# Optimization experiments

Measured on AMD Instinct MI355X. Metric: run time of the kernel, lower is better.

## Reference

```python
import jax, jax.numpy as jnp
import numpy as np

TAU = 0.07          # temperature
TOP_N_SIM = 5       # n_neighb for KNN label assignment
RANKING_K = 4       # top-k same/diff-class sims for confidence ratio


def setup_inputs() -> dict:
    key = jax.random.key(0)
    k1, k2, k3 = jax.random.split(key, 3)
    n_src, n_tgt, d, n_cls = 8192, 6144, 256, 64
    return {
        "source_features": jax.random.normal(k1, (n_src, d), dtype=jnp.float32),
        "source_labels": jax.random.randint(k2, (n_src,), 0, n_cls, dtype=jnp.int32),
        "target_features": jax.random.normal(k3, (n_tgt, d), dtype=jnp.float32),
    }


def _l2_normalize(x):
    # F.normalize(x, dim=1, p=2) with eps=1e-12
    n = jnp.sqrt(jnp.sum(x * x, axis=1, keepdims=True))
    return x / jnp.maximum(n, 1e-12)


def reference(source_features, source_labels, target_features):
    n_tgt = target_features.shape[0]
    top_ranked_n = n_tgt * 2 // 3

    # cosine similarity matrix [n_src, n_tgt]
    sim = _l2_normalize(source_features) @ _l2_normalize(target_features).T

    # sort each column descending over sources
    order = jnp.argsort(-sim, axis=0)                      # [S, T]

    # KNN label assignment with torch.mode semantics (tie -> smallest value)
    neigh = source_labels[order[:TOP_N_SIM]]               # [K, T]
    counts = (neigh[:, None, :] == neigh[None, :, :]).sum(axis=1)  # [K, T]
    maxc = counts.max(axis=0)                              # [T]
    big = jnp.iinfo(source_labels.dtype).max
    assigned = jnp.where(counts == maxc[None, :], neigh, big).min(axis=0)  # [T]

    # sims & labels reordered by descending similarity, per column
    sorted_sims = jnp.take_along_axis(sim, order, axis=0)  # [S, T]
    sorted_labels = source_labels[order]                   # [S, T]
    pos = sorted_labels == assigned[None, :]               # [S, T]

    def first_k_masked_sum(mask):
        # sum of first RANKING_K sorted sims where mask is True, per column
        csum = jnp.cumsum(mask.astype(sim.dtype), axis=0)
        sel = mask & (csum <= RANKING_K)
        return jnp.sum(jnp.where(sel, sorted_sims, 0.0), axis=0)

    nln = first_k_masked_sum(pos)
    nun = first_k_masked_sum(~pos)
    scores = jax.lax.stop_gradient(nln / nun)              # [T], detached

    _, top_ind = jax.lax.top_k(scores, top_ranked_n)       # confident targets
    conf_sim = sim[:, top_ind]                             # [S, top_ranked_n]
    conf_lab = assigned[top_ind]

    # contrastive softmax loss over sources
    mask_sim = (source_labels[:, None] == conf_lab[None, :]).astype(sim.dtype)
    exp_scores = jax.nn.softmax(conf_sim / TAU, axis=0)
    contrastive = (exp_scores * mask_sim).sum(axis=0) / exp_scores.sum(axis=0)
    return -jnp.mean(jnp.log(contrastive + 1e-6))
```

## Files before the change

kernel.cpp:

```cpp
#include <hip/hip_runtime.h>
#include <cstdint>
#include <cstddef>

#define DIM 256
#define NSRC 8192
#define NTGT 6144
#define NCLS 64
#define KSTEPS 8
#define INV_TAU (1.0f / 0.07f)
#define EPITCH 136

typedef __attribute__((ext_vector_type(8))) short bf16x8;
typedef __attribute__((ext_vector_type(4))) float f32x4;
typedef unsigned char uchar;

__device__ __forceinline__ ushort f2bf_rne(float f) {
    uint u = __float_as_uint(f);
    uint r = u + 0x7fff + ((u >> 16) & 1);
    return (ushort)(r >> 16);
}
__device__ __forceinline__ uint bf2ord(uint u) {
    return u ^ (0x8000u + (u >> 15) * 0x7FFFu);
}
__device__ __forceinline__ float ord2f(uint o) {
    uint u = (o & 0x8000u) ? (o ^ 0x8000u) : (~o & 0xFFFFu);
    return __uint_as_float(u << 16);
}
__device__ __forceinline__ uint med3u(uint a, uint b, uint c) {
    uint d;
    asm("v_med3_u32 %0, %1, %2, %3" : "=v"(d) : "v"(a), "v"(b), "v"(c));
    return d;
}

__device__ __forceinline__ void gload_lds16(const void* g, void* l) {
    __builtin_amdgcn_global_load_lds((const __attribute__((address_space(1))) void*)g,
                                     (__attribute__((address_space(3))) void*)l,
                                     16, 0, 0);
}

__global__ __launch_bounds__(256) void l2bf2_k(const float* __restrict__ inA,
                                               ushort* __restrict__ outA, int nA,
                                               const float* __restrict__ inB,
                                               ushort* __restrict__ outB, int nB) {
    const int w = (blockIdx.x * 256 + threadIdx.x) >> 6;
    const int lane = threadIdx.x & 63;
    if (w >= nA + nB) return;
    const float* in;
    ushort* out;
    int row;
    if (w < nA) { in = inA; out = outA; row = w; }
    else        { in = inB; out = outB; row = w - nA; }
    float4 v = *(const float4*)(in + (size_t)row * DIM + lane * 4);
    float ss = v.x * v.x + v.y * v.y + v.z * v.z + v.w * v.w;
#pragma unroll
    for (int d = 1; d < 64; d <<= 1) ss += __shfl_xor(ss, d);
    const float n = fmaxf(sqrtf(ss), 1e-12f);
    ushort4 o;
    o.x = f2bf_rne(v.x / n);
    o.y = f2bf_rne(v.y / n);
    o.z = f2bf_rne(v.z / n);
    o.w = f2bf_rne(v.w / n);
    *(ushort4*)(out + (size_t)row * DIM + lane * 4) = o;
}

__global__ __launch_bounds__(256) void class_build_k(const int* __restrict__ labels,
                                                     uchar* __restrict__ lab8,
                                                     int* __restrict__ cstart,
                                                     int* __restrict__ clist, int n) {
    const int c = blockIdx.x, t = threadIdx.x;
    const int g = c * 256 + t;
    if (g < n) lab8[g] = (uchar)labels[g];

    __shared__ int sl[256], se[256];
    const int per = n >> 8;
    const int i0 = t * per;
    int less = 0, eq = 0;
    for (int j = 0; j < per; ++j) {
        const int l = labels[i0 + j];
        less += (l < c);
        eq += (l == c);
    }
    sl[t] = less; se[t] = eq;
    __syncthreads();
    for (int s = 1; s < 256; s <<= 1) {
        const int a = (t >= s) ? sl[t - s] : 0;
        const int b = (t >= s) ? se[t - s] : 0;
        __syncthreads();
        sl[t] += a; se[t] += b;
        __syncthreads();
    }
    const int base = sl[255];
    int pos = base + se[t] - eq;
    for (int j = 0; j < per; ++j) {
        const int i = i0 + j;
        if (labels[i] == c) clist[pos++] = i;
    }
    if (t == 0) cstart[c] = base;
    if (c == 0 && t == 1) cstart[NCLS] = n;
}

__global__ __launch_bounds__(256) void gemm_mfma_k(const ushort* __restrict__ A,
                                                   const ushort* __restrict__ B,
                                                   ushort* __restrict__ C,
                                                   float* __restrict__ s1p,
                                                   int M, int N) {
    __shared__ __align__(16) ushort smem[24576];

    const int tid = threadIdx.x;
    const int lane = tid & 63, wid = tid >> 6;
    const int wr = wid >> 1, wc = wid & 1;

    const int gx = gridDim.x;
    const int bid = blockIdx.y * gx + blockIdx.x;
    const int rowsPerX = gridDim.y >> 3;
    const int grpW = 8;
    const int grpSize = rowsPerX * grpW;
    const int xcd = bid & 7;
    const int local = bid >> 3;
    const int grp = local / grpSize;
    const int within = local % grpSize;
    const int bm = (xcd * rowsPerX + within % rowsPerX) * 128;
    const int bn = (grp * grpW + within / rowsPerX) * 128;

    const char* aSrc[2];
    const char* bSrc[2];
    uint ldsOff[2];
#pragma unroll
    for (int it = 0; it < 2; ++it) {
        const int c = it * 256 + tid;
        const int r = c >> 2;
        const int ch = c & 3;
        const int sch = ch ^ ((r >> 1) & 3);
        aSrc[it] = (const char*)A + (size_t)(bm + r) * (DIM * 2) + sch * 16;
        bSrc[it] = (const char*)B + (size_t)(bn + r) * (DIM * 2) + sch * 16;
        ldsOff[it] = it * 4096 + (uint)(wid * 1024);
    }

    const int fr = lane & 15, fk = lane >> 4;
    const int swz = (fr >> 1) & 3;
    int idxA[4], idxB[4];
#pragma unroll
    for (int m = 0; m < 4; ++m)
        idxA[m] = (wr * 64 + m * 16 + fr) * 32 + ((fk ^ swz) * 8);
#pragma unroll
    for (int n = 0; n < 4; ++n)
        idxB[n] = (wc * 64 + n * 16 + fr) * 32 + ((fk ^ swz) * 8);

    f32x4 acc[4][4];
#pragma unroll
    for (int m = 0; m < 4; ++m)
#pragma unroll
        for (int n = 0; n < 4; ++n) acc[m][n] = (f32x4){0.f, 0.f, 0.f, 0.f};

#define STAGE(b, ks)                                                               \
    {                                                                              \
        _Pragma("unroll") for (int it = 0; it < 2; ++it) {                         \
            gload_lds16(aSrc[it] + (ks) * 64,                                      \
                        (char*)smem + (b) * 8192 + ldsOff[it]);                    \
            gload_lds16(bSrc[it] + (ks) * 64,                                      \
                        (char*)smem + 24576 + (b) * 8192 + ldsOff[it]);            \
        }                                                                          \
    }

    STAGE(0, 0);
    STAGE(1, 1);

#pragma unroll
    for (int ks = 0; ks < KSTEPS; ++ks) {
        if (ks < KSTEPS - 1) { asm volatile("s_waitcnt vmcnt(4)" ::: "memory"); }
        else                 { asm volatile("s_waitcnt vmcnt(0)" ::: "memory"); }
        __builtin_amdgcn_s_barrier();
        asm volatile("" ::: "memory");

        if (ks + 2 < KSTEPS) STAGE((ks + 2) % 3, ks + 2);

        const int slot = ks % 3;
        const ushort* sAc = smem + slot * 4096;
        const ushort* sBc = smem + 12288 + slot * 4096;
        bf16x8 av[4], bv[4];
#pragma unroll
        for (int m = 0; m < 4; ++m) av[m] = *(const bf16x8*)&sAc[idxA[m]];
#pragma unroll
        for (int n = 0; n < 4; ++n) bv[n] = *(const bf16x8*)&sBc[idxB[n]];
#pragma unroll
        for (int m = 0; m < 4; ++m)
#pragma unroll
            for (int n = 0; n < 4; ++n)
                acc[m][n] = __builtin_amdgcn_mfma_f32_16x16x32_bf16(av[m], bv[n], acc[m][n], 0, 0, 0);
    }
#undef STAGE

    __syncthreads();
    {
        float rp[16];
#pragma unroll
        for (int m = 0; m < 4; ++m)
#pragma unroll
            for (int j = 0; j < 4; ++j) {
                float s = 0.f;
#pragma unroll
                for (int n = 0; n < 4; ++n) {
                    uint u = __float_as_uint(acc[m][n][j]);
                    uint ru = (u + 0x7fff + ((u >> 16) & 1)) & 0xFFFF0000u;
                    s += __expf(fmaf(__uint_as_float(ru), INV_TAU, -INV_TAU));
                }
                rp[m * 4 + j] = s;
            }
#pragma unroll
        for (int d = 1; d < 16; d <<= 1)
#pragma unroll
            for (int i = 0; i < 16; ++i) rp[i] += __shfl_xor(rp[i], d);
        float* s1red = (float*)((char*)smem + 34816);
        if (fr == 0) {
#pragma unroll
            for (int m = 0; m < 4; ++m)
#pragma unroll
                for (int j = 0; j < 4; ++j)
                    s1red[(wr * 64 + m * 16 + fk * 4 + j) * 2 + wc] = rp[m * 4 + j];
        }
    }
#pragma unroll
    for (int m = 0; m < 4; ++m) {
#pragma unroll
        for (int n = 0; n < 4; ++n) {
            const int colb = wc * 64 + n * 16 + fr;
#pragma unroll
            for (int j = 0; j < 4; ++j) {
                const int rowb = wr * 64 + m * 16 + fk * 4 + j;
                smem[rowb * EPITCH + colb] = (ushort)bf2ord((uint)f2bf_rne(acc[m][n][j]));
            }
        }
    }
    __syncthreads();
    if (tid < 128) {
        const float* s1red = (const float*)((const char*)smem + 34816);
        s1p[(size_t)(bn >> 7) * NTGT + bm + tid] = s1red[tid * 2] + s1red[tid * 2 + 1];
    }
    const int rr = tid >> 4, cc = (tid & 15) * 8;
#pragma unroll
    for (int it = 0; it < 8; ++it) {
        const int r = it * 16 + rr;
        uint4 v = *(const uint4*)&smem[r * EPITCH + cc];
        *(uint4*)(C + (size_t)(bm + r) * N + bn + cc) = v;
    }
}

__global__ __launch_bounds__(256) void assign_score_w(const ushort* __restrict__ sim,
                                                      const int* __restrict__ labels,
                                                      const uchar* __restrict__ lab8,
                                                      const int* __restrict__ cstart,
                                                      const int* __restrict__ clist,
                                                      const float* __restrict__ s1p,
                                                      float* __restrict__ scores_out,
                                                      float* __restrict__ logt_out) {
    const int lane = threadIdx.x & 63, wid = threadIdx.x >> 6;
    const int t = blockIdx.x * 4 + wid;
    const ushort* row = sim + (size_t)t * NSRC;

    uint k0 = 0, k1 = 0, k2 = 0, k3 = 0, k4 = 0, k5 = 0, k6 = 0, k7 = 0;

#define CH4(u16, idx)                                                   \
    {                                                                   \
        uint nk = (((uint)(u16)) << 16) | (uint)(8191 - (idx));         \
        uint q1 = med3u(nk, k0, k1);                                    \
        uint q2 = med3u(nk, k1, k2);                                    \
        uint q3 = med3u(nk, k2, k3);                                    \
        k0 = max(k0, nk); k1 = q1; k2 = q2; k3 = q3;                    \
    }
#define CH8(u16, idx)                                                   \
    {                                                                   \
        uint nk = (((uint)(u16)) << 16) | (uint)(8191 - (idx));         \
        uint q1 = med3u(nk, k0, k1);                                    \
        uint q2 = med3u(nk, k1, k2);                                    \
        uint q3 = med3u(nk, k2, k3);                                    \
        uint q4 = med3u(nk, k3, k4);                                    \
        uint q5 = med3u(nk, k4, k5);                                    \
        uint q6 = med3u(nk, k5, k6);                                    \
        uint q7 = med3u(nk, k6, k7);                                    \
        k0 = max(k0, nk);                                               \
        k1 = q1; k2 = q2; k3 = q3; k4 = q4; k5 = q5; k6 = q6; k7 = q7;  \
    }
#define MERGE8                                                                     \
    _Pragma("unroll")                                                              \
    for (int d = 1; d < 64; d <<= 1) {                                             \
        uint b0 = __shfl_xor(k0, d), b1 = __shfl_xor(k1, d), b2 = __shfl_xor(k2, d),\
             b3 = __shfl_xor(k3, d), b4 = __shfl_xor(k4, d), b5 = __shfl_xor(k5, d),\
             b6 = __shfl_xor(k6, d), b7 = __shfl_xor(k7, d);                        \
        uint r0 = max(k0, b0);                                                     \
        uint r1 = max(max(min(k0, b0), k1), b1);                                   \
        uint r2 = max(max(min(k0, b1), min(k1, b0)), max(k2, b2));                 \
        uint r3 = max(max(min(k0, b2), min(k1, b1)),                               \
                      max(max(min(k2, b0), k3), b3));                              \
        uint r4 = max(max(max(min(k0, b3), min(k1, b2)),                           \
                          max(min(k2, b1), min(k3, b0))), max(k4, b4));            \
        uint r5 = max(max(max(min(k0, b4), min(k1, b3)),                           \
                          max(min(k2, b2), min(k3, b1))),                          \
                      max(max(min(k4, b0), k5), b5));                              \
        uint r6 = max(max(max(min(k0, b5), min(k1, b4)),                           \
                          max(min(k2, b3), min(k3, b2))),                          \
                      max(max(min(k4, b1), min(k5, b0)), max(k6, b6)));            \
        uint r7 = max(max(max(min(k0, b6), min(k1, b5)),                           \
                          max(min(k2, b4), min(k3, b3))),                          \
                      max(max(min(k4, b2), min(k5, b1)),                           \
                          max(max(min(k6, b0), k7), b7)));                         \
        k0 = r0; k1 = r1; k2 = r2; k3 = r3; k4 = r4; k5 = r5; k6 = r6; k7 = r7;    \
    }

    for (int i0 = lane * 8; i0 < NSRC; i0 += 512) {
        uint4 w = *(const uint4*)(row + i0);
        CH4(w.x & 0xFFFF, i0 + 0); CH4(w.x >> 16, i0 + 1);
        CH4(w.y & 0xFFFF, i0 + 2); CH4(w.y >> 16, i0 + 3);
        CH4(w.z & 0xFFFF, i0 + 4); CH4(w.z >> 16, i0 + 5);
        CH4(w.w & 0xFFFF, i0 + 6); CH4(w.w >> 16, i0 + 7);
    }
    const uint prek3 = k3;
    MERGE8;
    if (!__all((int)(prek3 <= k7))) {
        k0 = k1 = k2 = k3 = k4 = k5 = k6 = k7 = 0;
        for (int i0 = lane * 8; i0 < NSRC; i0 += 512) {
            uint4 w = *(const uint4*)(row + i0);
            CH8(w.x & 0xFFFF, i0 + 0); CH8(w.x >> 16, i0 + 1);
            CH8(w.y & 0xFFFF, i0 + 2); CH8(w.y >> 16, i0 + 3);
            CH8(w.z & 0xFFFF, i0 + 4); CH8(w.z >> 16, i0 + 5);
            CH8(w.w & 0xFFFF, i0 + 6); CH8(w.w >> 16, i0 + 7);
        }
        MERGE8;
    }
#undef CH4
#undef CH8
#undef MERGE8

    float s1 = s1p[(size_t)lane * NTGT + t];
#pragma unroll
    for (int d = 1; d < 64; d <<= 1) s1 += __shfl_xor(s1, d);

    const int l0 = labels[8191 - (int)(k0 & 0xFFFF)];
    const int l1 = labels[8191 - (int)(k1 & 0xFFFF)];
    const int l2 = labels[8191 - (int)(k2 & 0xFFFF)];
    const int l3 = labels[8191 - (int)(k3 & 0xFFFF)];
    const int l4 = labels[8191 - (int)(k4 & 0xFFFF)];
    const int l5 = labels[8191 - (int)(k5 & 0xFFFF)];
    const int l6 = labels[8191 - (int)(k6 & 0xFFFF)];
    const int l7 = labels[8191 - (int)(k7 & 0xFFFF)];

    const int c0 = 1 + (l0 == l1) + (l0 == l2) + (l0 == l3) + (l0 == l4);
    const int c1 = (l1 == l0) + 1 + (l1 == l2) + (l1 == l3) + (l1 == l4);
    const int c2 = (l2 == l0) + (l2 == l1) + 1 + (l2 == l3) + (l2 == l4);
    const int c3 = (l3 == l0) + (l3 == l1) + (l3 == l2) + 1 + (l3 == l4);
    const int c4 = (l4 == l0) + (l4 == l1) + (l4 == l2) + (l4 == l3) + 1;
    const int maxc = max(max(max(c0, c1), max(c2, c3)), c4);
    int assigned = 0x7fffffff;
    if (c0 == maxc) assigned = min(assigned, l0);
    if (c1 == maxc) assigned = min(assigned, l1);
    if (c2 == maxc) assigned = min(assigned, l2);
    if (c3 == maxc) assigned = min(assigned, l3);
    if (c4 == maxc) assigned = min(assigned, l4);
    const int aL = assigned;

    const int negcnt = (l0 != aL) + (l1 != aL) + (l2 != aL) + (l3 != aL) +
                       (l4 != aL) + (l5 != aL) + (l6 != aL) + (l7 != aL);
    float nun = 0.f;
    if (negcnt >= 4) {
        int c = 0;
#define NSTEP(kj, lj)                                                       \
        {                                                                   \
            bool take = ((lj) != aL) && (c < 4);                            \
            nun += take ? ord2f((kj) >> 16) : 0.f;                          \
            c += take ? 1 : 0;                                              \
        }
        NSTEP(k0, l0) NSTEP(k1, l1) NSTEP(k2, l2) NSTEP(k3, l3)
        NSTEP(k4, l4) NSTEP(k5, l5) NSTEP(k6, l6) NSTEP(k7, l7)
#undef NSTEP
    } else {
        uint n0 = 0, n1 = 0, n2 = 0, n3 = 0;
        for (int i0 = lane * 8; i0 < NSRC; i0 += 512) {
            uint4 w = *(const uint4*)(row + i0);
            uint2 lw = *(const uint2*)(lab8 + i0);
#define NEGP(u16, lb)                                                       \
            {                                                               \
                uint x = ((lb) == aL) ? 0u : (uint)(u16);                   \
                uint q1 = med3u(x, n0, n1);                                 \
                uint q2 = med3u(x, n1, n2);                                 \
                uint q3 = med3u(x, n2, n3);                                 \
                n0 = max(n0, x); n1 = q1; n2 = q2; n3 = q3;                 \
            }
            NEGP(w.x & 0xFFFF, (int)(lw.x & 255));
            NEGP(w.x >> 16,    (int)((lw.x >> 8) & 255));
            NEGP(w.y & 0xFFFF, (int)((lw.x >> 16) & 255));
            NEGP(w.y >> 16,    (int)(lw.x >> 24));
            NEGP(w.z & 0xFFFF, (int)(lw.y & 255));
            NEGP(w.z >> 16,    (int)((lw.y >> 8) & 255));
            NEGP(w.w & 0xFFFF, (int)((lw.y >> 16) & 255));
            NEGP(w.w >> 16,    (int)(lw.y >> 24));
#undef NEGP
        }
#pragma unroll
        for (int d = 1; d < 64; d <<= 1) {
            uint b0 = __shfl_xor(n0, d), b1 = __shfl_xor(n1, d),
                 b2 = __shfl_xor(n2, d), b3 = __shfl_xor(n3, d);
            uint r0 = max(n0, b0);
            uint r1 = max(max(min(n0, b0), n1), b1);
            uint r2 = max(max(min(n0, b1), min(n1, b0)), max(n2, b2));
            uint r3 = max(max(min(n0, b2), min(n1, b1)),
                          max(max(min(n2, b0), n3), b3));
            n0 = r0; n1 = r1; n2 = r2; n3 = r3;
        }
        nun = (n0 ? ord2f(n0) : 0.f) + (n1 ? ord2f(n1) : 0.f) +
              (n2 ? ord2f(n2) : 0.f) + (n3 ? ord2f(n3) : 0.f);
    }

    const int cs = cstart[aL], ce = cstart[aL + 1];
    float tp0 = -2.f, tp1 = -2.f, tp2 = -2.f, tp3 = -2.f;
    float sp = 0.f;
    for (int p = cs + lane; p < ce; p += 64) {
        const int idx = clist[p];
        float v = ord2f((uint)row[idx]);
        sp += __expf(fmaf(v, INV_TAU, -INV_TAU));
        float q1 = __builtin_amdgcn_fmed3f(v, tp0, tp1);
        float q2 = __builtin_amdgcn_fmed3f(v, tp1, tp2);
        float q3 = __builtin_amdgcn_fmed3f(v, tp2, tp3);
        tp0 = fmaxf(tp0, v); tp1 = q1; tp2 = q2; tp3 = q3;
    }
#pragma unroll
    for (int d = 1; d < 64; d <<= 1) {
        sp += __shfl_xor(sp, d);
        float b0 = __shfl_xor(tp0, d), b1 = __shfl_xor(tp1, d),
              b2 = __shfl_xor(tp2, d), b3 = __shfl_xor(tp3, d);
        float r0 = fmaxf(tp0, b0);
        float r1 = fmaxf(fmaxf(fminf(tp0, b0), tp1), b1);
        float r2 = fmaxf(fmaxf(fminf(tp0, b1), fminf(tp1, b0)), fmaxf(tp2, b2));
        float r3 = fmaxf(fmaxf(fminf(tp0, b2), fminf(tp1, b1)),
                         fmaxf(fmaxf(fminf(tp2, b0), tp3), b3));
        tp0 = r0; tp1 = r1; tp2 = r2; tp3 = r3;
    }

    if (lane == 0) {
        float nln = (tp0 > -1.5f ? tp0 : 0.f) + (tp1 > -1.5f ? tp1 : 0.f) +
                    (tp2 > -1.5f ? tp2 : 0.f) + (tp3 > -1.5f ? tp3 : 0.f);
        scores_out[t] = nln / nun;
        logt_out[t] = logf(sp / s1 + 1e-6f);
    }
}

__global__ __launch_bounds__(256) void select_topk_w(const float* __restrict__ scores,
                                                     int* __restrict__ selected,
                                                     int n, int k) {
    const int lane = threadIdx.x & 63, wid = threadIdx.x >> 6;
    const int t = blockIdx.x * 4 + wid;
    if (t >= n) return;
    const float st = scores[t];
    int rank = 0;
    for (int j0 = lane * 4; j0 < n; j0 += 256) {
        float4 v = *(const float4*)(scores + j0);
        rank += (v.x > st) || (v.x == st && (j0 + 0) < t);
        rank += (v.y > st) || (v.y == st && (j0 + 1) < t);
        rank += (v.z > st) || (v.z == st && (j0 + 2) < t);
        rank += (v.w > st) || (v.w == st && (j0 + 3) < t);
    }
    for (int d = 1; d < 64; d <<= 1) rank += __shfl_xor(rank, d);
    if (lane == 0) selected[t] = (rank < k) ? 1 : 0;
}

__global__ __launch_bounds__(256) void finalize_k(const float* __restrict__ logt,
                                                  const int* __restrict__ selected,
                                                  float* __restrict__ out, int n, int k) {
    __shared__ float red[256];
    const int tid = threadIdx.x;
    float s = 0.f;
    for (int i = tid; i < n; i += 256) s += selected[i] ? logt[i] : 0.f;
    red[tid] = s;
    __syncthreads();
    for (int st = 128; st > 0; st >>= 1) {
        if (tid < st) red[tid] += red[tid + st];
        __syncthreads();
    }
    if (tid == 0) out[0] = -red[0] / (float)k;
}

extern "C" void kernel_launch(void* const* d_in, const int* in_sizes, int n_in,
                              void* d_out, int out_size, void* d_ws, size_t ws_size,
                              hipStream_t stream) {
    const float* srcF = (const float*)d_in[0];
    const int* labels = (const int*)d_in[1];
    const float* tgtF = (const float*)d_in[2];
    float* out = (float*)d_out;

    const int n_src = in_sizes[1];
    const int d = in_sizes[0] / n_src;
    const int n_tgt = in_sizes[2] / d;
    const int topn = n_tgt * 2 / 3;

    char* ws = (char*)d_ws;
    ushort* src2 = (ushort*)ws;  ws += (size_t)n_src * DIM * sizeof(ushort);
    ushort* tgt2 = (ushort*)ws;  ws += (size_t)n_tgt * DIM * sizeof(ushort);
    ushort* sim  = (ushort*)ws;  ws += (size_t)n_tgt * NSRC * sizeof(ushort);
    float* scores = (float*)ws;  ws += (size_t)n_tgt * sizeof(float);
    float* logt   = (float*)ws;  ws += (size_t)n_tgt * sizeof(float);
    int* selected = (int*)ws;    ws += (size_t)n_tgt * sizeof(int);
    int* cstart   = (int*)ws;    ws += (size_t)(NCLS + 1) * sizeof(int);
    int* clist    = (int*)ws;    ws += (size_t)n_src * sizeof(int);
    uchar* lab8   = (uchar*)ws;  ws += (size_t)n_src;
    ws = (char*)(((uintptr_t)ws + 255) & ~(uintptr_t)255);
    float* s1p    = (float*)ws;  ws += (size_t)64 * NTGT * sizeof(float);

    const int nrows = n_tgt + n_src;
    l2bf2_k<<<(nrows + 3) / 4, 256, 0, stream>>>(tgtF, tgt2, n_tgt, srcF, src2, n_src);
    class_build_k<<<NCLS, 256, 0, stream>>>(labels, lab8, cstart, clist, n_src);

    dim3 grid(n_src / 128, n_tgt / 128);
    gemm_mfma_k<<<grid, 256, 0, stream>>>(tgt2, src2, sim, s1p, n_tgt, n_src);

    assign_score_w<<<n_tgt / 4, 256, 0, stream>>>(sim, labels, lab8, cstart, clist,
                                                  s1p, scores, logt);
    select_topk_w<<<(n_tgt + 3) / 4, 256, 0, stream>>>(scores, selected, n_tgt, topn);
    finalize_k<<<1, 256, 0, stream>>>(logt, selected, out, n_tgt, topn);
}
```

Before: 128.3 us.

## Move exp-sum from GEMM epilogue into assign kernel, store raw bf16

Drops the per-tile exp-sum reduction and the s1p partial-sum buffer from the GEMM epilogue. The softmax denominator is now computed in the assign kernel while it already streams each row. The GEMM stores plain bf16 instead of order-preserving keys, and the key transform moves into the assign kernel's selection loops. The main loop now handles two independent 512-element chunks with separate top-4 lists that are merged afterwards, to raise ILP. This takes work off the GEMM epilogue and removes a global buffer, but the assign kernel must now do an exp and a key transform per element.

```diff
diff --git a/kernel.cpp b/kernel.cpp
--- a/kernel.cpp
+++ b/kernel.cpp
@@ -4,7 +4,6 @@
 
 #define DIM 256
 #define NSRC 8192
-#define NTGT 6144
 #define NCLS 64
 #define KSTEPS 8
 #define INV_TAU (1.0f / 0.07f)
@@ -102,7 +101,6 @@
 __global__ __launch_bounds__(256) void gemm_mfma_k(const ushort* __restrict__ A,
                                                    const ushort* __restrict__ B,
                                                    ushort* __restrict__ C,
-                                                   float* __restrict__ s1p,
                                                    int M, int N) {
     __shared__ __align__(16) ushort smem[24576];
 
@@ -191,34 +189,6 @@
 #undef STAGE
 
     __syncthreads();
-    {
-        float rp[16];
-#pragma unroll
-        for (int m = 0; m < 4; ++m)
-#pragma unroll
-            for (int j = 0; j < 4; ++j) {
-                float s = 0.f;
-#pragma unroll
-                for (int n = 0; n < 4; ++n) {
-                    uint u = __float_as_uint(acc[m][n][j]);
-                    uint ru = (u + 0x7fff + ((u >> 16) & 1)) & 0xFFFF0000u;
-                    s += __expf(fmaf(__uint_as_float(ru), INV_TAU, -INV_TAU));
-                }
-                rp[m * 4 + j] = s;
-            }
-#pragma unroll
-        for (int d = 1; d < 16; d <<= 1)
-#pragma unroll
-            for (int i = 0; i < 16; ++i) rp[i] += __shfl_xor(rp[i], d);
-        float* s1red = (float*)((char*)smem + 34816);
-        if (fr == 0) {
-#pragma unroll
-            for (int m = 0; m < 4; ++m)
-#pragma unroll
-                for (int j = 0; j < 4; ++j)
-                    s1red[(wr * 64 + m * 16 + fk * 4 + j) * 2 + wc] = rp[m * 4 + j];
-        }
-    }
 #pragma unroll
     for (int m = 0; m < 4; ++m) {
 #pragma unroll
@@ -227,15 +197,11 @@
 #pragma unroll
             for (int j = 0; j < 4; ++j) {
                 const int rowb = wr * 64 + m * 16 + fk * 4 + j;
-                smem[rowb * EPITCH + colb] = (ushort)bf2ord((uint)f2bf_rne(acc[m][n][j]));
+                smem[rowb * EPITCH + colb] = f2bf_rne(acc[m][n][j]);
             }
         }
     }
     __syncthreads();
-    if (tid < 128) {
-        const float* s1red = (const float*)((const char*)smem + 34816);
-        s1p[(size_t)(bn >> 7) * NTGT + bm + tid] = s1red[tid * 2] + s1red[tid * 2 + 1];
-    }
     const int rr = tid >> 4, cc = (tid & 15) * 8;
 #pragma unroll
     for (int it = 0; it < 8; ++it) {
@@ -250,26 +216,33 @@
                                                       const uchar* __restrict__ lab8,
                                                       const int* __restrict__ cstart,
                                                       const int* __restrict__ clist,
-                                                      const float* __restrict__ s1p,
                                                       float* __restrict__ scores_out,
                                                       float* __restrict__ logt_out) {
     const int lane = threadIdx.x & 63, wid = threadIdx.x >> 6;
     const int t = blockIdx.x * 4 + wid;
     const ushort* row = sim + (size_t)t * NSRC;
 
-    uint k0 = 0, k1 = 0, k2 = 0, k3 = 0, k4 = 0, k5 = 0, k6 = 0, k7 = 0;
-
-#define CH4(u16, idx)                                                   \
+    uint kA0 = 0, kA1 = 0, kA2 = 0, kA3 = 0;
+    uint kB0 = 0, kB1 = 0, kB2 = 0, kB3 = 0;
+    float s1a = 0.f, s1b = 0.f;
+
+#define CH4X(u16, idx, K0, K1, K2, K3, S1)                              \
     {                                                                   \
-        uint nk = (((uint)(u16)) << 16) | (uint)(8191 - (idx));         \
-        uint q1 = med3u(nk, k0, k1);                                    \
-        uint q2 = med3u(nk, k1, k2);                                    \
-        uint q3 = med3u(nk, k2, k3);                                    \
-        k0 = max(k0, nk); k1 = q1; k2 = q2; k3 = q3;                    \
+        uint uu = (uint)(u16);                                          \
+        float vv = __uint_as_float(uu << 16);                           \
+        S1 += __expf(fmaf(vv, INV_TAU, -INV_TAU));                      \
+        uint od = uu ^ (0x8000u + (uu >> 15) * 0x7FFFu);                \
+        uint nk = (od << 16) | (uint)(8191 - (idx));                    \
+        uint q1 = med3u(nk, K0, K1);                                    \
+        uint q2 = med3u(nk, K1, K2);                                    \
+        uint q3 = med3u(nk, K2, K3);                                    \
+        K0 = max(K0, nk); K1 = q1; K2 = q2; K3 = q3;                    \
     }
 #define CH8(u16, idx)                                                   \
     {                                                                   \
-        uint nk = (((uint)(u16)) << 16) | (uint)(8191 - (idx));         \
+        uint uu = (uint)(u16);                                          \
+        uint od = uu ^ (0x8000u + (uu >> 15) * 0x7FFFu);                \
+        uint nk = (od << 16) | (uint)(8191 - (idx));                    \
         uint q1 = med3u(nk, k0, k1);                                    \
         uint q2 = med3u(nk, k1, k2);                                    \
         uint q3 = med3u(nk, k2, k3);                                    \
@@ -306,13 +279,33 @@
         k0 = r0; k1 = r1; k2 = r2; k3 = r3; k4 = r4; k5 = r5; k6 = r6; k7 = r7;    \
     }
 
-    for (int i0 = lane * 8; i0 < NSRC; i0 += 512) {
+    for (int i0 = lane * 8; i0 < NSRC; i0 += 1024) {
         uint4 w = *(const uint4*)(row + i0);
-        CH4(w.x & 0xFFFF, i0 + 0); CH4(w.x >> 16, i0 + 1);
-        CH4(w.y & 0xFFFF, i0 + 2); CH4(w.y >> 16, i0 + 3);
-        CH4(w.z & 0xFFFF, i0 + 4); CH4(w.z >> 16, i0 + 5);
-        CH4(w.w & 0xFFFF, i0 + 6); CH4(w.w >> 16, i0 + 7);
-    }
+        uint4 w2 = *(const uint4*)(row + i0 + 512);
+        CH4X(w.x & 0xFFFF, i0 + 0, kA0, kA1, kA2, kA3, s1a);
+        CH4X(w.x >> 16,    i0 + 1, kA0, kA1, kA2, kA3, s1a);
+        CH4X(w.y & 0xFFFF, i0 + 2, kA0, kA1, kA2, kA3, s1a);
+        CH4X(w.y >> 16,    i0 + 3, kA0, kA1, kA2, kA3, s1a);
+        CH4X(w.z & 0xFFFF, i0 + 4, kA0, kA1, kA2, kA3, s1a);
+        CH4X(w.z >> 16,    i0 + 5, kA0, kA1, kA2, kA3, s1a);
+        CH4X(w.w & 0xFFFF, i0 + 6, kA0, kA1, kA2, kA3, s1a);
+        CH4X(w.w >> 16,    i0 + 7, kA0, kA1, kA2, kA3, s1a);
+        CH4X(w2.x & 0xFFFF, i0 + 512, kB0, kB1, kB2, kB3, s1b);
+        CH4X(w2.x >> 16,    i0 + 513, kB0, kB1, kB2, kB3, s1b);
+        CH4X(w2.y & 0xFFFF, i0 + 514, kB0, kB1, kB2, kB3, s1b);
+        CH4X(w2.y >> 16,    i0 + 515, kB0, kB1, kB2, kB3, s1b);
+        CH4X(w2.z & 0xFFFF, i0 + 516, kB0, kB1, kB2, kB3, s1b);
+        CH4X(w2.z >> 16,    i0 + 517, kB0, kB1, kB2, kB3, s1b);
+        CH4X(w2.w & 0xFFFF, i0 + 518, kB0, kB1, kB2, kB3, s1b);
+        CH4X(w2.w >> 16,    i0 + 519, kB0, kB1, kB2, kB3, s1b);
+    }
+    uint k0 = max(kA0, kB0);
+    uint k1 = max(max(min(kA0, kB0), kA1), kB1);
+    uint k2 = max(max(min(kA0, kB1), min(kA1, kB0)), max(kA2, kB2));
+    uint k3 = max(max(min(kA0, kB2), min(kA1, kB1)),
+                  max(max(min(kA2, kB0), kA3), kB3));
+    uint k4 = 0, k5 = 0, k6 = 0, k7 = 0;
+
     const uint prek3 = k3;
     MERGE8;
     if (!__all((int)(prek3 <= k7))) {
@@ -326,11 +319,11 @@
         }
         MERGE8;
     }
-#undef CH4
+#undef CH4X
 #undef CH8
 #undef MERGE8
 
-    float s1 = s1p[(size_t)lane * NTGT + t];
+    float s1 = s1a + s1b;
 #pragma unroll
     for (int d = 1; d < 64; d <<= 1) s1 += __shfl_xor(s1, d);
 
@@ -378,7 +371,9 @@
             uint2 lw = *(const uint2*)(lab8 + i0);
 #define NEGP(u16, lb)                                                       \
             {                                                               \
-                uint x = ((lb) == aL) ? 0u : (uint)(u16);                   \
+                uint uu = (uint)(u16);                                      \
+                uint od = uu ^ (0x8000u + (uu >> 15) * 0x7FFFu);            \
+                uint x = ((lb) == aL) ? 0u : od;                            \
                 uint q1 = med3u(x, n0, n1);                                 \
                 uint q2 = med3u(x, n1, n2);                                 \
                 uint q3 = med3u(x, n2, n3);                                 \
@@ -414,7 +409,7 @@
     float sp = 0.f;
     for (int p = cs + lane; p < ce; p += 64) {
         const int idx = clist[p];
-        float v = ord2f((uint)row[idx]);
+        float v = __uint_as_float(((uint)row[idx]) << 16);
         sp += __expf(fmaf(v, INV_TAU, -INV_TAU));
         float q1 = __builtin_amdgcn_fmed3f(v, tp0, tp1);
         float q2 = __builtin_amdgcn_fmed3f(v, tp1, tp2);
@@ -500,18 +495,16 @@
     int* cstart   = (int*)ws;    ws += (size_t)(NCLS + 1) * sizeof(int);
     int* clist    = (int*)ws;    ws += (size_t)n_src * sizeof(int);
     uchar* lab8   = (uchar*)ws;  ws += (size_t)n_src;
-    ws = (char*)(((uintptr_t)ws + 255) & ~(uintptr_t)255);
-    float* s1p    = (float*)ws;  ws += (size_t)64 * NTGT * sizeof(float);
 
     const int nrows = n_tgt + n_src;
     l2bf2_k<<<(nrows + 3) / 4, 256, 0, stream>>>(tgtF, tgt2, n_tgt, srcF, src2, n_src);
     class_build_k<<<NCLS, 256, 0, stream>>>(labels, lab8, cstart, clist, n_src);
 
     dim3 grid(n_src / 128, n_tgt / 128);
-    gemm_mfma_k<<<grid, 256, 0, stream>>>(tgt2, src2, sim, s1p, n_tgt, n_src);
+    gemm_mfma_k<<<grid, 256, 0, stream>>>(tgt2, src2, sim, n_tgt, n_src);
 
     assign_score_w<<<n_tgt / 4, 256, 0, stream>>>(sim, labels, lab8, cstart, clist,
-                                                  s1p, scores, logt);
+                                                  scores, logt);
     select_topk_w<<<(n_tgt + 3) / 4, 256, 0, stream>>>(scores, selected, n_tgt, topn);
     finalize_k<<<1, 256, 0, stream>>>(logt, selected, out, n_tgt, topn);
 }
```

After: 109.2 us. 1.17x faster.
